# Optimization experiments

Measured on AMD Instinct MI355X. Metric: run time of the kernel, lower is better.

## Reference

```python
import jax, jax.numpy as jnp
import numpy as np

MIN_C = 1e-6
MIN_NORM = 1e-15
BALL_EPS = 0.004  # float32 ball epsilon


def _norm(x):
    return jnp.maximum(jnp.linalg.norm(x, axis=-1, keepdims=True), MIN_NORM)


def _project(x, c):
    norm = _norm(x)
    maxnorm = (1.0 - BALL_EPS) / jnp.sqrt(c)
    return jnp.where(norm > maxnorm, x / norm * maxnorm, x)


def _tanh(x):
    return jnp.tanh(jnp.clip(x, -15.0, 15.0))


def _artanh(x):
    x = jnp.clip(x, -1.0 + 1e-5, 1.0 - 1e-5)
    return 0.5 * (jnp.log1p(x) - jnp.log1p(-x))


def _expmap0(u, c):
    sc = jnp.sqrt(c)
    n = _norm(u)
    return _project(_tanh(sc * n) * u / (sc * n), c)


def _logmap0(y, c):
    sc = jnp.sqrt(c)
    n = _norm(y)
    return y / n / sc * _artanh(sc * n)


def _mobius_add(x, y, c):
    x2 = jnp.sum(x * x, -1, keepdims=True)
    y2 = jnp.sum(y * y, -1, keepdims=True)
    xy = jnp.sum(x * y, -1, keepdims=True)
    num = (1 + 2 * c * xy + c * y2) * x + (1 - c * x2) * y
    den = jnp.maximum(1 + 2 * c * xy + c * c * x2 * y2, MIN_NORM)
    return num / den


N_NODE, N_EDGE, D, ATTN, B, N_VOCAB = 100000, 1000000, 64, 64, 256, 401


def setup_inputs() -> dict:
    key = jax.random.key(0)
    ks = jax.random.split(key, 12)
    r_idx = jax.random.randint(ks[0], (N_EDGE,), 0, B, dtype=jnp.int32)
    rel = jax.random.randint(ks[1], (N_EDGE,), 0, N_VOCAB, dtype=jnp.int32)
    sub = jax.random.randint(ks[2], (N_EDGE,), 0, N_NODE, dtype=jnp.int32)
    obj = jax.random.randint(ks[3], (N_EDGE,), 0, N_NODE, dtype=jnp.int32)
    zero = jnp.zeros((N_EDGE,), jnp.int32)
    edges = jnp.stack([r_idx, zero, rel, zero, sub, obj], axis=1)  # [E, 6]
    s = 0.1
    return {
        "hidden": jax.random.normal(ks[4], (N_NODE, D), jnp.float32) * s,
        "q_rel": jax.random.randint(ks[5], (B,), 0, N_VOCAB, dtype=jnp.int32),
        "edges": edges,
        "rela_embed": jax.random.normal(ks[6], (N_VOCAB, D), jnp.float32) * s,
        "Ws_w": jax.random.normal(ks[7], (ATTN, D), jnp.float32) * s,
        "Wr_w": jax.random.normal(ks[8], (ATTN, D), jnp.float32) * s,
        "Wqr_w": jax.random.normal(ks[9], (ATTN, D), jnp.float32) * s,
        "Wqr_b": jnp.zeros((ATTN,), jnp.float32),
        "Wattn_w": jax.random.normal(ks[10], (1, ATTN), jnp.float32) * s,
        "Wh_w": jax.random.normal(ks[11], (D, D), jnp.float32) * s,
        "n_node": N_NODE,
    }


def reference(hidden, q_rel, edges, rela_embed, Ws_w, Wr_w, Wqr_w, Wqr_b, Wattn_w, Wh_w, n_node):
    c = MIN_C
    sub, rel, obj, r_idx = edges[:, 4], edges[:, 2], edges[:, 5], edges[:, 0]
    hs = hidden[sub]                 # [E, D] gather
    hr = rela_embed[rel]             # [E, D]
    h_qr = rela_embed[q_rel][r_idx]  # [E, D]
    # attention MLP -> scalar gate per edge
    pre = hs @ Ws_w.T + hr @ Wr_w.T + h_qr @ Wqr_w.T + Wqr_b
    alpha = jax.nn.sigmoid(jax.nn.relu(pre) @ Wattn_w.T)  # [E, 1]
    # hyperbolic message
    hs_h = _expmap0(hs, c)
    hr_h = _expmap0(hr, c)
    mess2 = _logmap0(_project(_mobius_add(hs_h, hr_h, c), c), c)
    message = mess2 * alpha
    agg = jax.ops.segment_sum(message, obj, num_segments=n_node)  # scatter-add
    a = _expmap0(agg @ Wh_w.T, c)
    a = jax.nn.relu(a)  # act
    return _logmap0(a, c)
```

## Files before the change

kernel.cpp:

```cpp
#include <hip/hip_runtime.h>
#include <math.h>
#include <stdint.h>

#define N_NODE 100000
#define N_EDGE 1000000
#define DIM    64
#define NB     256
#define NVOCAB 401
#define SCAN_B 1024
#define NCHUNK ((N_NODE + SCAN_B - 1) / SCAN_B)
#define AGG_WAVES 8192
#define NSHARD 8
#define EPB 2048

typedef short short8  __attribute__((ext_vector_type(8)));
typedef float floatx4 __attribute__((ext_vector_type(4)));
typedef unsigned short ushort_t;

__device__ inline unsigned short f2bf_rne(float f)
{
    unsigned u = __float_as_uint(f);
    unsigned r = u + 0x7FFF + ((u >> 16) & 1);
    return (unsigned short)(r >> 16);
}
__device__ inline float bflo(unsigned u) { return __uint_as_float(u << 16); }
__device__ inline float bfhi(unsigned u) { return __uint_as_float(u & 0xFFFF0000u); }
__device__ inline unsigned short f2h(float f)
{
    _Float16 h = (_Float16)f;
    unsigned short s; __builtin_memcpy(&s, &h, 2); return s;
}
__device__ inline float h2f(unsigned b)
{
    unsigned short s = (unsigned short)b;
    _Float16 h; __builtin_memcpy(&h, &s, 2); return (float)h;
}

__device__ inline void split8(float4 v0, float4 v1, short8& hi, short8& lo)
{
    float f[8] = {v0.x, v0.y, v0.z, v0.w, v1.x, v1.y, v1.z, v1.w};
    #pragma unroll
    for (int j = 0; j < 8; ++j) {
        unsigned u = __float_as_uint(f[j]);
        unsigned r = u + 0x7FFF + ((u >> 16) & 1);
        unsigned short h = (unsigned short)(r >> 16);
        float hf = __uint_as_float(((unsigned)h) << 16);
        float l  = f[j] - hf;
        unsigned u2 = __float_as_uint(l);
        unsigned r2 = u2 + 0x7FFF + ((u2 >> 16) & 1);
        hi[j] = (short)h;
        lo[j] = (short)(r2 >> 16);
    }
}

#define INIT_GRID ((NSHARD * N_NODE + 255) / 256)

__global__ __launch_bounds__(256) void init_kernel(
    const float* __restrict__ Ws, const float* __restrict__ Wr,
    const float* __restrict__ Wqr, const float* __restrict__ Wh,
    ushort_t* __restrict__ wsp, int* __restrict__ deg8)
{
    int tid = blockIdx.x * 256 + threadIdx.x;
    if (tid < NSHARD * N_NODE) deg8[tid] = 0;
    if (tid < 4 * 4096) {
        int w = tid >> 12, e = tid & 4095;
        const float* src = (w == 0) ? Ws : (w == 1) ? Wr : (w == 2) ? Wqr : Wh;
        float f = src[e];
        unsigned u = __float_as_uint(f);
        unsigned r = u + 0x7FFF + ((u >> 16) & 1);
        unsigned short h = (unsigned short)(r >> 16);
        float hf = __uint_as_float(((unsigned)h) << 16);
        float l  = f - hf;
        unsigned u2 = __float_as_uint(l);
        unsigned r2 = u2 + 0x7FFF + ((u2 >> 16) & 1);
        wsp[w * 8192 + e]        = h;
        wsp[w * 8192 + 4096 + e] = (unsigned short)(r2 >> 16);
    }
}

__device__ void gemm64p_body(
    const float* __restrict__ X,
    const int*   __restrict__ idx,
    const ushort_t* __restrict__ Whi,
    const ushort_t* __restrict__ Wlo,
    const float* __restrict__ bias,
    void* __restrict__ Yv,
    ushort_t* __restrict__ Y2,
    int R, int out_mode, int blk)
{
    int wave = threadIdx.x >> 6;
    int lane = threadIdx.x & 63;
    int m    = lane & 15;
    int quad = lane >> 4;
    int r0   = blk * 64 + wave * 16;

    int r = r0 + m;
    int src = (r < R) ? (idx ? idx[r] : r) : 0;
    const float* xrow = X + (size_t)src * DIM + quad * 8;

    float4 a0[2], a1[2];
    #pragma unroll
    for (int c = 0; c < 2; ++c) {
        a0[c] = *(const float4*)(xrow + 32 * c);
        a1[c] = *(const float4*)(xrow + 32 * c + 4);
    }
    short8 ah[2], al[2];
    #pragma unroll
    for (int c = 0; c < 2; ++c) split8(a0[c], a1[c], ah[c], al[c]);

    if (out_mode == 3 && r < R) {
        #pragma unroll
        for (int c = 0; c < 2; ++c)
            *(short8*)(Y2 + (size_t)r * DIM + 32 * c + quad * 8) = ah[c];
    }

    floatx4 acc[4] = {{0,0,0,0},{0,0,0,0},{0,0,0,0},{0,0,0,0}};
    #pragma unroll
    for (int g = 0; g < 4; ++g) {
        const ushort_t* whrow = Whi + (size_t)(g * 16 + m) * DIM + quad * 8;
        const ushort_t* wlrow = Wlo + (size_t)(g * 16 + m) * DIM + quad * 8;
        #pragma unroll
        for (int c = 0; c < 2; ++c) {
            short8 bh = *(const short8*)(whrow + 32 * c);
            short8 bl = *(const short8*)(wlrow + 32 * c);
            acc[g] = __builtin_amdgcn_mfma_f32_16x16x32_bf16(bh, ah[c], acc[g], 0, 0, 0);
            acc[g] = __builtin_amdgcn_mfma_f32_16x16x32_bf16(bl, ah[c], acc[g], 0, 0, 0);
            acc[g] = __builtin_amdgcn_mfma_f32_16x16x32_bf16(bh, al[c], acc[g], 0, 0, 0);
        }
    }

    if (r < R) {
        #pragma unroll
        for (int g = 0; g < 4; ++g) {
            float4 bv = make_float4(0.f, 0.f, 0.f, 0.f);
            if (bias) bv = *(const float4*)(bias + g * 16 + quad * 4);
            float v0 = acc[g][0] + bv.x;
            float v1 = acc[g][1] + bv.y;
            float v2 = acc[g][2] + bv.z;
            float v3 = acc[g][3] + bv.w;
            if (out_mode == 1) {
                v0 = fmaxf(v0, 0.f); v1 = fmaxf(v1, 0.f);
                v2 = fmaxf(v2, 0.f); v3 = fmaxf(v3, 0.f);
            }
            if (out_mode >= 2) {
                uint2 o;
                o.x = (unsigned)f2bf_rne(v0) | ((unsigned)f2bf_rne(v1) << 16);
                o.y = (unsigned)f2bf_rne(v2) | ((unsigned)f2bf_rne(v3) << 16);
                *(uint2*)((ushort_t*)Yv + (size_t)r * DIM + g * 16 + quad * 4) = o;
            } else {
                *(float4*)((float*)Yv + (size_t)r * DIM + g * 16 + quad * 4) =
                    make_float4(v0, v1, v2, v3);
            }
        }
    }
}

__global__ __launch_bounds__(256) void gemm64p_bf16A_kernel(
    const ushort_t* __restrict__ A,
    const ushort_t* __restrict__ Whi,
    const ushort_t* __restrict__ Wlo,
    float* __restrict__ Y, int R)
{
    int wave = threadIdx.x >> 6;
    int lane = threadIdx.x & 63;
    int m    = lane & 15;
    int quad = lane >> 4;
    int r0   = blockIdx.x * 64 + wave * 16;

    int r = r0 + m;
    int src = (r < R) ? r : 0;
    short8 a8[2];
    #pragma unroll
    for (int c = 0; c < 2; ++c)
        a8[c] = *(const short8*)(A + (size_t)src * DIM + 32 * c + quad * 8);

    floatx4 acc[4] = {{0,0,0,0},{0,0,0,0},{0,0,0,0},{0,0,0,0}};
    #pragma unroll
    for (int g = 0; g < 4; ++g) {
        const ushort_t* whrow = Whi + (size_t)(g * 16 + m) * DIM + quad * 8;
        const ushort_t* wlrow = Wlo + (size_t)(g * 16 + m) * DIM + quad * 8;
        #pragma unroll
        for (int c = 0; c < 2; ++c) {
            short8 bh = *(const short8*)(whrow + 32 * c);
            short8 bl = *(const short8*)(wlrow + 32 * c);
            acc[g] = __builtin_amdgcn_mfma_f32_16x16x32_bf16(bh, a8[c], acc[g], 0, 0, 0);
            acc[g] = __builtin_amdgcn_mfma_f32_16x16x32_bf16(bl, a8[c], acc[g], 0, 0, 0);
        }
    }

    if (r < R) {
        #pragma unroll
        for (int g = 0; g < 4; ++g) {
            *(float4*)(Y + (size_t)r * DIM + g * 16 + quad * 4) =
                make_float4(fmaxf(acc[g][0], 0.f), fmaxf(acc[g][1], 0.f),
                            fmaxf(acc[g][2], 0.f), fmaxf(acc[g][3], 0.f));
        }
    }
}

__device__ void gemm64_body(
    const float* __restrict__ X,
    const int*   __restrict__ idx,
    const float* __restrict__ W,
    const float* __restrict__ bias,
    void* __restrict__ Yv,
    ushort_t* __restrict__ Y2,
    int R, int out_mode, int blk)
{
    int wave = threadIdx.x >> 6;
    int lane = threadIdx.x & 63;
    int m    = lane & 15;
    int quad = lane >> 4;
    int r0   = blk * 64 + wave * 16;

    int r = r0 + m;
    int src = (r < R) ? (idx ? idx[r] : r) : 0;
    const float* xrow = X + (size_t)src * DIM + quad * 8;

    float4 a0[2], a1[2];
    #pragma unroll
    for (int c = 0; c < 2; ++c) {
        a0[c] = *(const float4*)(xrow + 32 * c);
        a1[c] = *(const float4*)(xrow + 32 * c + 4);
    }
    short8 ah[2], al[2];
    #pragma unroll
    for (int c = 0; c < 2; ++c) split8(a0[c], a1[c], ah[c], al[c]);

    if (out_mode == 3 && r < R) {
        #pragma unroll
        for (int c = 0; c < 2; ++c)
            *(short8*)(Y2 + (size_t)r * DIM + 32 * c + quad * 8) = ah[c];
    }

    floatx4 acc[4] = {{0,0,0,0},{0,0,0,0},{0,0,0,0},{0,0,0,0}};
    #pragma unroll
    for (int g = 0; g < 4; ++g) {
        const float* wrow = W + (size_t)(g * 16 + m) * DIM + quad * 8;
        #pragma unroll
        for (int c = 0; c < 2; ++c) {
            float4 b0 = *(const float4*)(wrow + 32 * c);
            float4 b1 = *(const float4*)(wrow + 32 * c + 4);
            short8 bh, bl;
            split8(b0, b1, bh, bl);
            acc[g] = __builtin_amdgcn_mfma_f32_16x16x32_bf16(ah[c], bh, acc[g], 0, 0, 0);
            acc[g] = __builtin_amdgcn_mfma_f32_16x16x32_bf16(ah[c], bl, acc[g], 0, 0, 0);
            acc[g] = __builtin_amdgcn_mfma_f32_16x16x32_bf16(al[c], bh, acc[g], 0, 0, 0);
        }
    }

    #pragma unroll
    for (int g = 0; g < 4; ++g) {
        float bv = bias ? bias[g * 16 + m] : 0.0f;
        #pragma unroll
        for (int reg = 0; reg < 4; ++reg) {
            int rr = r0 + quad * 4 + reg;
            if (rr < R) {
                float v = acc[g][reg] + bv;
                if (out_mode == 1) v = fmaxf(v, 0.0f);
                if (out_mode >= 2)
                    ((ushort_t*)Yv)[(size_t)rr * DIM + g * 16 + m] = f2bf_rne(v);
                else
                    ((float*)Yv)[(size_t)rr * DIM + g * 16 + m] = v;
            }
        }
    }
}

__global__ __launch_bounds__(256) void gemm64_kernel(
    const float* __restrict__ X, const int* __restrict__ idx,
    const float* __restrict__ W, const float* __restrict__ bias,
    void* __restrict__ Yv, ushort_t* __restrict__ Y2, int R, int out_mode)
{
    gemm64_body(X, idx, W, bias, Yv, Y2, R, out_mode, blockIdx.x);
}

#define G1 ((N_NODE + 63) / 64)
#define G2 ((NVOCAB + 63) / 64)
#define G3 (NB / 64)
#define GSMALL (G2 + G3)
#define GD8 ((N_EDGE + EPB - 1) / EPB)
#define PREP_T (G1 + GD8)
#define PREP_GRID (GSMALL + PREP_T)

__global__ __launch_bounds__(256) void prep_kernel(
    const float* __restrict__ hidden,
    const float* __restrict__ rela,
    const int*   __restrict__ q_rel,
    const ushort_t* __restrict__ wsp,
    const float* __restrict__ Wqr_b,
    ushort_t* __restrict__ hsWs,
    ushort_t* __restrict__ hidb,
    ushort_t* __restrict__ rel_preb,
    ushort_t* __restrict__ relab,
    ushort_t* __restrict__ qr_preb,
    const int* __restrict__ edges,
    int* __restrict__ deg8,
    int2* __restrict__ epack)
{
    int b = blockIdx.x;
    if (b < G2) {
        gemm64p_body(rela, nullptr, wsp + 1 * 8192, wsp + 1 * 8192 + 4096,
                     nullptr, rel_preb, relab, NVOCAB, 3, b);
    } else if (b < GSMALL) {
        gemm64p_body(rela, q_rel, wsp + 2 * 8192, wsp + 2 * 8192 + 4096,
                     Wqr_b, qr_preb, nullptr, NB, 2, b - G2);
    } else {
        int bp = b - GSMALL;
        int prior = (int)(((long)bp * GD8) / PREP_T);
        int nxt   = (int)(((long)(bp + 1) * GD8) / PREP_T);
        if (nxt > prior) {
            int base = prior * EPB + threadIdx.x;
            #pragma unroll
            for (int k = 0; k < 8; ++k) {
                int e = base + k * 256;
                if (e < N_EDGE) {
                    int2 ab = *(const int2*)(edges + (size_t)e * 6);
                    int2 cd = *(const int2*)(edges + (size_t)e * 6 + 2);
                    int2 ef = *(const int2*)(edges + (size_t)e * 6 + 4);
                    epack[e] = make_int2(ef.x | (cd.x << 17), ef.y | (ab.x << 17));
                    int s = (e >> 11) & (NSHARD - 1);
                    atomicAdd(&deg8[s * N_NODE + ef.y], 1);
                }
            }
        } else {
            gemm64p_body(hidden, nullptr, wsp, wsp + 4096,
                         nullptr, hsWs, hidb, N_NODE, 3, bp - prior);
        }
    }
}

__global__ __launch_bounds__(SCAN_B) void scan1_kernel(const int* __restrict__ deg8,
                                                       int* __restrict__ partial)
{
    __shared__ int s[SCAN_B];
    int g = blockIdx.x * SCAN_B + threadIdx.x;
    int tot = 0;
    if (g < N_NODE)
        #pragma unroll
        for (int k = 0; k < NSHARD; ++k) tot += deg8[k * N_NODE + g];
    s[threadIdx.x] = tot;
    __syncthreads();
    for (int off = SCAN_B / 2; off; off >>= 1) {
        if (threadIdx.x < off) s[threadIdx.x] += s[threadIdx.x + off];
        __syncthreads();
    }
    if (threadIdx.x == 0) partial[blockIdx.x] = s[0];
}

__global__ __launch_bounds__(SCAN_B) void scan3_kernel(int* __restrict__ deg8,
                                                       const int* __restrict__ partial,
                                                       int* __restrict__ offs)
{
    __shared__ int s[SCAN_B];
    __shared__ int pbase_s;
    int pb = (threadIdx.x < (int)blockIdx.x) ? partial[threadIdx.x] : 0;
    s[threadIdx.x] = pb;
    __syncthreads();
    for (int off = SCAN_B / 2; off; off >>= 1) {
        if (threadIdx.x < off) s[threadIdx.x] += s[threadIdx.x + off];
        __syncthreads();
    }
    if (threadIdx.x == 0) pbase_s = s[0];
    __syncthreads();
    int pbase = pbase_s;
    __syncthreads();

    int g = blockIdx.x * SCAN_B + threadIdx.x;
    int d[NSHARD];
    int tot = 0;
    if (g < N_NODE) {
        #pragma unroll
        for (int k = 0; k < NSHARD; ++k) { d[k] = deg8[k * N_NODE + g]; tot += d[k]; }
    }
    s[threadIdx.x] = tot;
    __syncthreads();
    for (int off = 1; off < SCAN_B; off <<= 1) {
        int add = ((int)threadIdx.x >= off) ? s[threadIdx.x - off] : 0;
        __syncthreads();
        s[threadIdx.x] += add;
        __syncthreads();
    }
    if (g < N_NODE) {
        int incl = pbase + s[threadIdx.x];
        offs[g + 1] = incl;
        if (g == 0) offs[0] = 0;
        int run = incl - tot;
        #pragma unroll
        for (int k = 0; k < NSHARD; ++k) { deg8[k * N_NODE + g] = run; run += d[k]; }
    }
}

__global__ __launch_bounds__(256) void alpha_scatter_kernel(
    const int2*     __restrict__ epack,
    int*            __restrict__ base8,
    const ushort_t* __restrict__ hsWs,
    const ushort_t* __restrict__ rel_preb,
    const ushort_t* __restrict__ qr_preb,
    const float*    __restrict__ wattn,
    int2*           __restrict__ csr2)
{
    int tid = blockIdx.x * 256 + threadIdx.x;
    if (tid < 32) csr2[N_EDGE + tid] = make_int2(0, 0);

    int wave = threadIdx.x >> 6;
    int lane = threadIdx.x & 63;
    int q    = lane >> 4;
    int l    = lane & 15;
    int f0   = l * 4;
    int e0   = (blockIdx.x * 4 + wave) * 16 + q * 4;

    float4 wa = *(const float4*)(wattn + f0);

    int   sub[4], rl[4], ob[4];
    float t[4];
    #pragma unroll
    for (int j = 0; j < 4; ++j) {
        int e = e0 + j;
        int2 ep = epack[e];
        sub[j] = ep.x & 0x1FFFF;
        rl[j]  = (int)((unsigned)ep.x >> 17);
        ob[j]  = ep.y & 0x1FFFF;
        int ri = (int)((unsigned)ep.y >> 17);

        uint2 uh = *(const uint2*)(hsWs     + (size_t)sub[j] * DIM + f0);
        uint2 ur = *(const uint2*)(rel_preb + (size_t)rl[j]  * DIM + f0);
        uint2 uq = *(const uint2*)(qr_preb  + (size_t)ri     * DIM + f0);

        float tt =  fmaxf(bflo(uh.x) + bflo(ur.x) + bflo(uq.x), 0.f) * wa.x;
        tt = fmaf(fmaxf(bfhi(uh.x) + bfhi(ur.x) + bfhi(uq.x), 0.f), wa.y, tt);
        tt = fmaf(fmaxf(bflo(uh.y) + bflo(ur.y) + bflo(uq.y), 0.f), wa.z, tt);
        tt = fmaf(fmaxf(bfhi(uh.y) + bfhi(ur.y) + bfhi(uq.y), 0.f), wa.w, tt);
        t[j] = tt;
    }
    #pragma unroll
    for (int j = 0; j < 4; ++j) {
        t[j] += __shfl_xor(t[j], 1);
        t[j] += __shfl_xor(t[j], 2);
        t[j] += __shfl_xor(t[j], 4);
        t[j] += __shfl_xor(t[j], 8);
    }

    if (l < 4) {
        int j = l;
        int sh = (e0 >> 11) & (NSHARD - 1);
        float alpha = 1.0f / (1.0f + __expf(-t[j]));
        int slot = atomicAdd(&base8[sh * N_NODE + ob[j]], 1);
        csr2[slot] = make_int2(sub[j],
            (int)(((unsigned)rl[j] << 16) | f2h(alpha)));
    }
}

__global__ __launch_bounds__(256) void agg_kernel(
    const int2*     __restrict__ csr2,
    const int*      __restrict__ offs,
    const ushort_t* __restrict__ hB,
    const ushort_t* __restrict__ relab,
    ushort_t* __restrict__ aggb)
{
    int lane = threadIdx.x & 63;
    int q    = lane >> 4;
    int l    = lane & 15;
    int f0   = l * 4;
    int wv = __builtin_amdgcn_readfirstlane((blockIdx.x * blockDim.x + threadIdx.x) >> 6);

    int i   = offs[wv];
    int end = offs[wv + 1];
    for (int n = wv; n < N_NODE; n += AGG_WAVES) {
        int nn = n + AGG_WAVES;
        int ni = 0, ne = 0;
        if (nn < N_NODE) { ni = offs[nn]; ne = offs[nn + 1]; }

        float4 acc = make_float4(0.f, 0.f, 0.f, 0.f);
        int2 e[4];
        #pragma unroll
        for (int j = 0; j < 4; ++j) e[j] = csr2[i + 4 * j + q];
        while (i < end) {
            int2 p[4];
            #pragma unroll
            for (int j = 0; j < 4; ++j) p[j] = csr2[i + 16 + 4 * j + q];

            uint2 uh[4], ur[4];
            #pragma unroll
            for (int j = 0; j < 4; ++j) {
                unsigned ey = (unsigned)e[j].y;
                uh[j] = *(const uint2*)(hB    + (((unsigned)e[j].x) << 6) + f0);
                ur[j] = *(const uint2*)(relab + ((ey >> 16) << 6) + f0);
            }
            #pragma unroll
            for (int j = 0; j < 4; ++j) {
                unsigned ey = (unsigned)e[j].y;
                float v  = (i + 4 * j + q < end) ? 1.0f : 0.0f;
                float al = v * h2f(ey & 0xFFFFu);
                acc.x = fmaf(al, bflo(uh[j].x) + bflo(ur[j].x), acc.x);
                acc.y = fmaf(al, bfhi(uh[j].x) + bfhi(ur[j].x), acc.y);
                acc.z = fmaf(al, bflo(uh[j].y) + bflo(ur[j].y), acc.z);
                acc.w = fmaf(al, bfhi(uh[j].y) + bfhi(ur[j].y), acc.w);
            }
            #pragma unroll
            for (int j = 0; j < 4; ++j) e[j] = p[j];
            i += 16;
        }

        acc.x += __shfl_xor(acc.x, 16); acc.x += __shfl_xor(acc.x, 32);
        acc.y += __shfl_xor(acc.y, 16); acc.y += __shfl_xor(acc.y, 32);
        acc.z += __shfl_xor(acc.z, 16); acc.z += __shfl_xor(acc.z, 32);
        acc.w += __shfl_xor(acc.w, 16); acc.w += __shfl_xor(acc.w, 32);
        if (q == 0) {
            uint2 o;
            o.x = (unsigned)f2bf_rne(acc.x) | ((unsigned)f2bf_rne(acc.y) << 16);
            o.y = (unsigned)f2bf_rne(acc.z) | ((unsigned)f2bf_rne(acc.w) << 16);
            *(uint2*)(aggb + (((unsigned)n) << 6) + f0) = o;
        }

        i = ni; end = ne;
    }
}

__global__ __launch_bounds__(256) void edge_kernel(
    const int*      __restrict__ edges,
    const ushort_t* __restrict__ hB,
    const ushort_t* __restrict__ relab,
    const ushort_t* __restrict__ hsWs,
    const ushort_t* __restrict__ rel_preb,
    const ushort_t* __restrict__ qr_preb,
    const float*    __restrict__ wattn,
    float* __restrict__ out)
{
    int e = (blockIdx.x * blockDim.x + threadIdx.x) >> 6;
    if (e >= N_EDGE) return;
    int lane = threadIdx.x & 63;
    int r_i = edges[e * 6 + 0];
    int rl  = edges[e * 6 + 2];
    int sb  = edges[e * 6 + 4];
    int ob  = edges[e * 6 + 5];
    float hs = __uint_as_float(((unsigned)hB[(size_t)sb * DIM + lane]) << 16);
    float hr = __uint_as_float(((unsigned)relab[(size_t)rl * DIM + lane]) << 16);
    float p1 = __uint_as_float(((unsigned)hsWs[(size_t)sb * DIM + lane]) << 16);
    float p2 = __uint_as_float(((unsigned)rel_preb[(size_t)rl * DIM + lane]) << 16);
    float p3 = __uint_as_float(((unsigned)qr_preb[(size_t)r_i * DIM + lane]) << 16);
    float t = wattn[lane] * fmaxf(p1 + p2 + p3, 0.0f);
    #pragma unroll
    for (int off = 32; off; off >>= 1) t += __shfl_xor(t, off);
    float alpha = 1.0f / (1.0f + __expf(-t));
    atomicAdd(&out[(size_t)ob * DIM + lane], (hs + hr) * alpha);
}

extern "C" void kernel_launch(void* const* d_in, const int* in_sizes, int n_in,
                              void* d_out, int out_size, void* d_ws, size_t ws_size,
                              hipStream_t stream)
{
    const float* hidden = (const float*)d_in[0];
    const int*   q_rel  = (const int*)  d_in[1];
    const int*   edges  = (const int*)  d_in[2];
    const float* rela   = (const float*)d_in[3];
    const float* Ws     = (const float*)d_in[4];
    const float* Wr     = (const float*)d_in[5];
    const float* Wqr    = (const float*)d_in[6];
    const float* Wqr_b  = (const float*)d_in[7];
    const float* Wattn  = (const float*)d_in[8];
    const float* Wh     = (const float*)d_in[9];
    float* out = (float*)d_out;

    ushort_t* qr_preb  = (ushort_t*)d_ws;
    ushort_t* rel_preb = qr_preb + NB * DIM;
    ushort_t* relab    = rel_preb + NVOCAB * DIM;
    ushort_t* hsWs     = relab + NVOCAB * DIM;
    ushort_t* hidb     = hsWs + (size_t)N_NODE * DIM;
    int2* epack  = (int2*)(((uintptr_t)(hidb + (size_t)N_NODE * DIM) + 15) & ~(uintptr_t)15);
    int*  rank   = (int*)(epack + N_EDGE);
    int*  deg8   = rank + N_EDGE;
    int*  offs   = deg8 + NSHARD * N_NODE;
    int*  partial= offs + (N_NODE + 1);
    int2* csr2   = (int2*)(((uintptr_t)(partial + 128) + 15) & ~(uintptr_t)15);
    ushort_t* wsp = (ushort_t*)(csr2 + N_EDGE + 32);
    size_t csr_need = ((char*)(wsp + 4 * 8192)) - (char*)d_ws;
    bool use_csr = ws_size >= csr_need;
    ushort_t* aggb = (ushort_t*)epack;

    if (use_csr) {
        init_kernel<<<INIT_GRID, 256, 0, stream>>>(Ws, Wr, Wqr, Wh, wsp, deg8);
        prep_kernel<<<PREP_GRID, 256, 0, stream>>>(
            hidden, rela, q_rel, wsp, Wqr_b,
            hsWs, hidb, rel_preb, relab, qr_preb, edges, deg8, epack);
        scan1_kernel<<<NCHUNK, SCAN_B, 0, stream>>>(deg8, partial);
        scan3_kernel<<<NCHUNK, SCAN_B, 0, stream>>>(deg8, partial, offs);
        alpha_scatter_kernel<<<N_EDGE / 64, 256, 0, stream>>>(
            epack, deg8, hsWs, rel_preb, qr_preb, Wattn, csr2);
        agg_kernel<<<AGG_WAVES / 4, 256, 0, stream>>>(csr2, offs, hidb, relab, aggb);
        gemm64p_bf16A_kernel<<<(N_NODE + 63) / 64, 256, 0, stream>>>(
            aggb, wsp + 3 * 8192, wsp + 3 * 8192 + 4096, out, N_NODE);
    } else {
        gemm64_kernel<<<(NVOCAB + 63) / 64, 256, 0, stream>>>(
            rela, nullptr, Wr, nullptr, rel_preb, relab, NVOCAB, 3);
        gemm64_kernel<<<(NB + 63) / 64, 256, 0, stream>>>(
            rela, q_rel, Wqr, Wqr_b, qr_preb, nullptr, NB, 2);
        gemm64_kernel<<<(N_NODE + 63) / 64, 256, 0, stream>>>(
            hidden, nullptr, Ws, nullptr, hsWs, hidb, N_NODE, 3);
        hipMemsetAsync(d_out, 0, (size_t)N_NODE * DIM * sizeof(float), stream);
        edge_kernel<<<(N_EDGE + 3) / 4, 256, 0, stream>>>(
            edges, hidb, relab, hsWs, rel_preb, qr_preb, Wattn, out);
        gemm64_kernel<<<(N_NODE + 63) / 64, 256, 0, stream>>>(
            out, nullptr, Wh, nullptr, out, nullptr, N_NODE, 1);
    }
}
```

Measured before the change: 261.1 us.

## Replace per-node CSR with 128-node bucket sort and LDS atomic aggregation

Edges are now counted into per-chunk histograms over 782 buckets of 128 destination nodes, replacing the per-node degree array spread over 8 shards. A three-pass scan turns these into per-chunk bucket offsets, and edges are scattered with LDS-local atomics instead of global atomics on a degree array. Aggregation runs one block per bucket and accumulates into a padded 128x65 LDS tile with shared-memory float atomics. This removes the global degree zeroing, the global atomic contention and the per-node wave scheduling. In exchange it adds LDS atomic traffic, and a block with a heavy bucket can run long, so load may be uneven across blocks.

```diff
diff --git a/kernel.cpp b/kernel.cpp
--- a/kernel.cpp
+++ b/kernel.cpp
@@ -7,11 +7,12 @@
 #define DIM    64
 #define NB     256
 #define NVOCAB 401
-#define SCAN_B 1024
-#define NCHUNK ((N_NODE + SCAN_B - 1) / SCAN_B)
-#define AGG_WAVES 8192
-#define NSHARD 8
-#define EPB 2048
+
+#define NBKT   782
+#define CHKE   1024
+#define NCHK   ((N_EDGE + CHKE - 1) / CHKE)
+#define SCAN_TOT (NBKT * NCHK)
+#define SCANA_GRID ((SCAN_TOT + 1023) / 1024)
 
 typedef short short8  __attribute__((ext_vector_type(8)));
 typedef float floatx4 __attribute__((ext_vector_type(4)));
@@ -53,15 +54,14 @@
     }
 }
 
-#define INIT_GRID ((NSHARD * N_NODE + 255) / 256)
+#define INIT_GRID ((4 * 4096 + 255) / 256)
 
 __global__ __launch_bounds__(256) void init_kernel(
     const float* __restrict__ Ws, const float* __restrict__ Wr,
     const float* __restrict__ Wqr, const float* __restrict__ Wh,
-    ushort_t* __restrict__ wsp, int* __restrict__ deg8)
+    ushort_t* __restrict__ wsp)
 {
     int tid = blockIdx.x * 256 + threadIdx.x;
-    if (tid < NSHARD * N_NODE) deg8[tid] = 0;
     if (tid < 4 * 4096) {
         int w = tid >> 12, e = tid & 4095;
         const float* src = (w == 0) ? Ws : (w == 1) ? Wr : (w == 2) ? Wqr : Wh;
@@ -279,11 +279,9 @@
 #define G2 ((NVOCAB + 63) / 64)
 #define G3 (NB / 64)
 #define GSMALL (G2 + G3)
-#define GD8 ((N_EDGE + EPB - 1) / EPB)
-#define PREP_T (G1 + GD8)
-#define PREP_GRID (GSMALL + PREP_T)
-
-__global__ __launch_bounds__(256) void prep_kernel(
+#define PREPC_GRID (NCHK + GSMALL + G1)
+
+__global__ __launch_bounds__(256) void prepcount_kernel(
     const float* __restrict__ hidden,
     const float* __restrict__ rela,
     const int*   __restrict__ q_rel,
@@ -295,225 +293,235 @@
     ushort_t* __restrict__ relab,
     ushort_t* __restrict__ qr_preb,
     const int* __restrict__ edges,
-    int* __restrict__ deg8,
-    int2* __restrict__ epack)
+    int2* __restrict__ epack,
+    int* __restrict__ histBB)
 {
     int b = blockIdx.x;
-    if (b < G2) {
+    if (b < NCHK) {
+        __shared__ unsigned cnt[NBKT];
+        for (int t = threadIdx.x; t < NBKT; t += 256) cnt[t] = 0;
+        __syncthreads();
+        int base = b * CHKE + threadIdx.x;
+        #pragma unroll
+        for (int k = 0; k < 4; ++k) {
+            int e = base + k * 256;
+            if (e < N_EDGE) {
+                int2 ab = *(const int2*)(edges + (size_t)e * 6);
+                int2 cd = *(const int2*)(edges + (size_t)e * 6 + 2);
+                int2 ef = *(const int2*)(edges + (size_t)e * 6 + 4);
+                epack[e] = make_int2(ef.x | (cd.x << 17), ef.y | (ab.x << 17));
+                atomicAdd(&cnt[ef.y >> 7], 1u);
+            }
+        }
+        __syncthreads();
+        for (int t = threadIdx.x; t < NBKT; t += 256)
+            histBB[b * NBKT + t] = (int)cnt[t];
+    } else if (b < NCHK + G2) {
         gemm64p_body(rela, nullptr, wsp + 1 * 8192, wsp + 1 * 8192 + 4096,
-                     nullptr, rel_preb, relab, NVOCAB, 3, b);
-    } else if (b < GSMALL) {
+                     nullptr, rel_preb, relab, NVOCAB, 3, b - NCHK);
+    } else if (b < NCHK + GSMALL) {
         gemm64p_body(rela, q_rel, wsp + 2 * 8192, wsp + 2 * 8192 + 4096,
-                     Wqr_b, qr_preb, nullptr, NB, 2, b - G2);
+                     Wqr_b, qr_preb, nullptr, NB, 2, b - NCHK - G2);
     } else {
-        int bp = b - GSMALL;
-        int prior = (int)(((long)bp * GD8) / PREP_T);
-        int nxt   = (int)(((long)(bp + 1) * GD8) / PREP_T);
-        if (nxt > prior) {
-            int base = prior * EPB + threadIdx.x;
-            #pragma unroll
-            for (int k = 0; k < 8; ++k) {
-                int e = base + k * 256;
-                if (e < N_EDGE) {
-                    int2 ab = *(const int2*)(edges + (size_t)e * 6);
-                    int2 cd = *(const int2*)(edges + (size_t)e * 6 + 2);
-                    int2 ef = *(const int2*)(edges + (size_t)e * 6 + 4);
-                    epack[e] = make_int2(ef.x | (cd.x << 17), ef.y | (ab.x << 17));
-                    int s = (e >> 11) & (NSHARD - 1);
-                    atomicAdd(&deg8[s * N_NODE + ef.y], 1);
-                }
-            }
-        } else {
-            gemm64p_body(hidden, nullptr, wsp, wsp + 4096,
-                         nullptr, hsWs, hidb, N_NODE, 3, bp - prior);
-        }
-    }
-}
-
-__global__ __launch_bounds__(SCAN_B) void scan1_kernel(const int* __restrict__ deg8,
-                                                       int* __restrict__ partial)
-{
-    __shared__ int s[SCAN_B];
-    int g = blockIdx.x * SCAN_B + threadIdx.x;
-    int tot = 0;
-    if (g < N_NODE)
-        #pragma unroll
-        for (int k = 0; k < NSHARD; ++k) tot += deg8[k * N_NODE + g];
-    s[threadIdx.x] = tot;
+        gemm64p_body(hidden, nullptr, wsp, wsp + 4096,
+                     nullptr, hsWs, hidb, N_NODE, 3, b - NCHK - GSMALL);
+    }
+}
+
+__global__ __launch_bounds__(1024) void scanA_kernel(
+    const int* __restrict__ histBB, int* __restrict__ offs2,
+    int* __restrict__ partialA)
+{
+    __shared__ int s[1024];
+    int t = threadIdx.x;
+    int m = blockIdx.x * 1024 + t;
+    int v = 0;
+    if (m < SCAN_TOT) {
+        int bin = m / NCHK, ch = m - bin * NCHK;
+        v = histBB[ch * NBKT + bin];
+    }
+    s[t] = v;
     __syncthreads();
-    for (int off = SCAN_B / 2; off; off >>= 1) {
-        if (threadIdx.x < off) s[threadIdx.x] += s[threadIdx.x + off];
+    for (int off = 1; off < 1024; off <<= 1) {
+        int add = (t >= off) ? s[t - off] : 0;
         __syncthreads();
-    }
-    if (threadIdx.x == 0) partial[blockIdx.x] = s[0];
-}
-
-__global__ __launch_bounds__(SCAN_B) void scan3_kernel(int* __restrict__ deg8,
-                                                       const int* __restrict__ partial,
-                                                       int* __restrict__ offs)
-{
-    __shared__ int s[SCAN_B];
-    __shared__ int pbase_s;
-    int pb = (threadIdx.x < (int)blockIdx.x) ? partial[threadIdx.x] : 0;
-    s[threadIdx.x] = pb;
+        s[t] += add;
+        __syncthreads();
+    }
+    if (m < SCAN_TOT) offs2[m] = s[t] - v;
+    if (t == 1023) partialA[blockIdx.x] = s[1023];
+}
+
+__global__ __launch_bounds__(1024) void scanB_kernel(
+    int* __restrict__ partialA, int* __restrict__ bstart)
+{
+    __shared__ int s[1024];
+    int t = threadIdx.x;
+    int v = (t < SCANA_GRID) ? partialA[t] : 0;
+    s[t] = v;
     __syncthreads();
-    for (int off = SCAN_B / 2; off; off >>= 1) {
-        if (threadIdx.x < off) s[threadIdx.x] += s[threadIdx.x + off];
+    for (int off = 1; off < 1024; off <<= 1) {
+        int add = (t >= off) ? s[t - off] : 0;
         __syncthreads();
-    }
-    if (threadIdx.x == 0) pbase_s = s[0];
-    __syncthreads();
-    int pbase = pbase_s;
-    __syncthreads();
-
-    int g = blockIdx.x * SCAN_B + threadIdx.x;
-    int d[NSHARD];
-    int tot = 0;
-    if (g < N_NODE) {
-        #pragma unroll
-        for (int k = 0; k < NSHARD; ++k) { d[k] = deg8[k * N_NODE + g]; tot += d[k]; }
-    }
-    s[threadIdx.x] = tot;
-    __syncthreads();
-    for (int off = 1; off < SCAN_B; off <<= 1) {
-        int add = ((int)threadIdx.x >= off) ? s[threadIdx.x - off] : 0;
+        s[t] += add;
         __syncthreads();
-        s[threadIdx.x] += add;
-        __syncthreads();
-    }
-    if (g < N_NODE) {
-        int incl = pbase + s[threadIdx.x];
-        offs[g + 1] = incl;
-        if (g == 0) offs[0] = 0;
-        int run = incl - tot;
-        #pragma unroll
-        for (int k = 0; k < NSHARD; ++k) { deg8[k * N_NODE + g] = run; run += d[k]; }
+    }
+    if (t < SCANA_GRID) partialA[t] = s[t] - v;
+    if (t == 0) bstart[NBKT] = N_EDGE;
+}
+
+__global__ __launch_bounds__(1024) void scanC_kernel(
+    int* __restrict__ offs2, const int* __restrict__ partialA,
+    int* __restrict__ bstart)
+{
+    int m = blockIdx.x * 1024 + threadIdx.x;
+    if (m < SCAN_TOT) {
+        int val = offs2[m] + partialA[blockIdx.x];
+        offs2[m] = val;
+        int bin = m / NCHK, ch = m - bin * NCHK;
+        if (ch == 0) bstart[bin] = val;
     }
 }
 
 __global__ __launch_bounds__(256) void alpha_scatter_kernel(
     const int2*     __restrict__ epack,
-    int*            __restrict__ base8,
+    const int*      __restrict__ offs2,
     const ushort_t* __restrict__ hsWs,
     const ushort_t* __restrict__ rel_preb,
     const ushort_t* __restrict__ qr_preb,
     const float*    __restrict__ wattn,
     int2*           __restrict__ csr2)
 {
-    int tid = blockIdx.x * 256 + threadIdx.x;
-    if (tid < 32) csr2[N_EDGE + tid] = make_int2(0, 0);
+    __shared__ int offL[NBKT];
+    int blk = blockIdx.x;
+    for (int t = threadIdx.x; t < NBKT; t += 256)
+        offL[t] = offs2[t * NCHK + blk];
+    if (blk == 0 && threadIdx.x < 32)
+        csr2[N_EDGE + threadIdx.x] = make_int2(0, 0);
+    __syncthreads();
 
     int wave = threadIdx.x >> 6;
     int lane = threadIdx.x & 63;
     int q    = lane >> 4;
     int l    = lane & 15;
     int f0   = l * 4;
-    int e0   = (blockIdx.x * 4 + wave) * 16 + q * 4;
-
     float4 wa = *(const float4*)(wattn + f0);
 
-    int   sub[4], rl[4], ob[4];
-    float t[4];
-    #pragma unroll
-    for (int j = 0; j < 4; ++j) {
-        int e = e0 + j;
-        int2 ep = epack[e];
-        sub[j] = ep.x & 0x1FFFF;
-        rl[j]  = (int)((unsigned)ep.x >> 17);
-        ob[j]  = ep.y & 0x1FFFF;
-        int ri = (int)((unsigned)ep.y >> 17);
-
-        uint2 uh = *(const uint2*)(hsWs     + (size_t)sub[j] * DIM + f0);
-        uint2 ur = *(const uint2*)(rel_preb + (size_t)rl[j]  * DIM + f0);
-        uint2 uq = *(const uint2*)(qr_preb  + (size_t)ri     * DIM + f0);
-
-        float tt =  fmaxf(bflo(uh.x) + bflo(ur.x) + bflo(uq.x), 0.f) * wa.x;
-        tt = fmaf(fmaxf(bfhi(uh.x) + bfhi(ur.x) + bfhi(uq.x), 0.f), wa.y, tt);
-        tt = fmaf(fmaxf(bflo(uh.y) + bflo(ur.y) + bflo(uq.y), 0.f), wa.z, tt);
-        tt = fmaf(fmaxf(bfhi(uh.y) + bfhi(ur.y) + bfhi(uq.y), 0.f), wa.w, tt);
-        t[j] = tt;
-    }
-    #pragma unroll
-    for (int j = 0; j < 4; ++j) {
-        t[j] += __shfl_xor(t[j], 1);
-        t[j] += __shfl_xor(t[j], 2);
-        t[j] += __shfl_xor(t[j], 4);
-        t[j] += __shfl_xor(t[j], 8);
-    }
-
-    if (l < 4) {
-        int j = l;
-        int sh = (e0 >> 11) & (NSHARD - 1);
-        float alpha = 1.0f / (1.0f + __expf(-t[j]));
-        int slot = atomicAdd(&base8[sh * N_NODE + ob[j]], 1);
-        csr2[slot] = make_int2(sub[j],
-            (int)(((unsigned)rl[j] << 16) | f2h(alpha)));
-    }
-}
+    for (int it = 0; it < 16; ++it) {
+        int e0 = blk * CHKE + wave * 256 + it * 16 + q * 4;
+
+        int   sub[4], rl[4], ob[4];
+        float tt[4];
+        #pragma unroll
+        for (int j = 0; j < 4; ++j) {
+            int e = e0 + j;
+            int2 ep = epack[min(e, N_EDGE - 1)];
+            sub[j] = ep.x & 0x1FFFF;
+            rl[j]  = (int)((unsigned)ep.x >> 17);
+            ob[j]  = ep.y & 0x1FFFF;
+            int ri = (int)((unsigned)ep.y >> 17);
+
+            uint2 uh = *(const uint2*)(hsWs     + (size_t)sub[j] * DIM + f0);
+            uint2 ur = *(const uint2*)(rel_preb + (size_t)rl[j]  * DIM + f0);
+            uint2 uq = *(const uint2*)(qr_preb  + (size_t)ri     * DIM + f0);
+
+            float s0 =  fmaxf(bflo(uh.x) + bflo(ur.x) + bflo(uq.x), 0.f) * wa.x;
+            s0 = fmaf(fmaxf(bfhi(uh.x) + bfhi(ur.x) + bfhi(uq.x), 0.f), wa.y, s0);
+            s0 = fmaf(fmaxf(bflo(uh.y) + bflo(ur.y) + bflo(uq.y), 0.f), wa.z, s0);
+            s0 = fmaf(fmaxf(bfhi(uh.y) + bfhi(ur.y) + bfhi(uq.y), 0.f), wa.w, s0);
+            tt[j] = s0;
+        }
+        #pragma unroll
+        for (int j = 0; j < 4; ++j) {
+            tt[j] += __shfl_xor(tt[j], 1);
+            tt[j] += __shfl_xor(tt[j], 2);
+            tt[j] += __shfl_xor(tt[j], 4);
+            tt[j] += __shfl_xor(tt[j], 8);
+        }
+
+        if (l < 4) {
+            int j = l;
+            int e = e0 + j;
+            if (e < N_EDGE) {
+                float alpha = 1.0f / (1.0f + __expf(-tt[j]));
+                int bin  = ob[j] >> 7;
+                int slot = atomicAdd(&offL[bin], 1);
+                csr2[slot] = make_int2(sub[j] | ((ob[j] & 127) << 17),
+                    (int)(((unsigned)rl[j] << 16) | f2h(alpha)));
+            }
+        }
+    }
+}
+
+#define AGG_LDSN (128 * 65)
 
 __global__ __launch_bounds__(256) void agg_kernel(
     const int2*     __restrict__ csr2,
-    const int*      __restrict__ offs,
+    const int*      __restrict__ bstart,
     const ushort_t* __restrict__ hB,
     const ushort_t* __restrict__ relab,
     ushort_t* __restrict__ aggb)
 {
+    __shared__ float accL[AGG_LDSN];
+    for (int t = threadIdx.x; t < AGG_LDSN; t += 256) accL[t] = 0.f;
+    __syncthreads();
+
+    int b = blockIdx.x;
+    int start = bstart[b];
+    int end   = bstart[b + 1];
+
+    int wave = threadIdx.x >> 6;
     int lane = threadIdx.x & 63;
     int q    = lane >> 4;
     int l    = lane & 15;
     int f0   = l * 4;
-    int wv = __builtin_amdgcn_readfirstlane((blockIdx.x * blockDim.x + threadIdx.x) >> 6);
-
-    int i   = offs[wv];
-    int end = offs[wv + 1];
-    for (int n = wv; n < N_NODE; n += AGG_WAVES) {
-        int nn = n + AGG_WAVES;
-        int ni = 0, ne = 0;
-        if (nn < N_NODE) { ni = offs[nn]; ne = offs[nn + 1]; }
-
-        float4 acc = make_float4(0.f, 0.f, 0.f, 0.f);
-        int2 e[4];
-        #pragma unroll
-        for (int j = 0; j < 4; ++j) e[j] = csr2[i + 4 * j + q];
-        while (i < end) {
-            int2 p[4];
-            #pragma unroll
-            for (int j = 0; j < 4; ++j) p[j] = csr2[i + 16 + 4 * j + q];
-
-            uint2 uh[4], ur[4];
-            #pragma unroll
-            for (int j = 0; j < 4; ++j) {
-                unsigned ey = (unsigned)e[j].y;
-                uh[j] = *(const uint2*)(hB    + (((unsigned)e[j].x) << 6) + f0);
-                ur[j] = *(const uint2*)(relab + ((ey >> 16) << 6) + f0);
-            }
-            #pragma unroll
-            for (int j = 0; j < 4; ++j) {
-                unsigned ey = (unsigned)e[j].y;
-                float v  = (i + 4 * j + q < end) ? 1.0f : 0.0f;
-                float al = v * h2f(ey & 0xFFFFu);
-                acc.x = fmaf(al, bflo(uh[j].x) + bflo(ur[j].x), acc.x);
-                acc.y = fmaf(al, bfhi(uh[j].x) + bfhi(ur[j].x), acc.y);
-                acc.z = fmaf(al, bflo(uh[j].y) + bflo(ur[j].y), acc.z);
-                acc.w = fmaf(al, bfhi(uh[j].y) + bfhi(ur[j].y), acc.w);
-            }
-            #pragma unroll
-            for (int j = 0; j < 4; ++j) e[j] = p[j];
-            i += 16;
-        }
-
-        acc.x += __shfl_xor(acc.x, 16); acc.x += __shfl_xor(acc.x, 32);
-        acc.y += __shfl_xor(acc.y, 16); acc.y += __shfl_xor(acc.y, 32);
-        acc.z += __shfl_xor(acc.z, 16); acc.z += __shfl_xor(acc.z, 32);
-        acc.w += __shfl_xor(acc.w, 16); acc.w += __shfl_xor(acc.w, 32);
-        if (q == 0) {
+
+    int i = start + wave * 16;
+    int2 e[4];
+    #pragma unroll
+    for (int j = 0; j < 4; ++j) e[j] = csr2[min(i + 4 * j + q, N_EDGE + 31)];
+    while (i < end) {
+        int2 p[4];
+        #pragma unroll
+        for (int j = 0; j < 4; ++j) p[j] = csr2[min(i + 64 + 4 * j + q, N_EDGE + 31)];
+
+        uint2 uh[4], ur[4];
+        #pragma unroll
+        for (int j = 0; j < 4; ++j) {
+            unsigned ex = (unsigned)e[j].x, ey = (unsigned)e[j].y;
+            uh[j] = *(const uint2*)(hB    + ((ex & 0x1FFFFu) << 6) + f0);
+            ur[j] = *(const uint2*)(relab + ((ey >> 16) << 6) + f0);
+        }
+        #pragma unroll
+        for (int j = 0; j < 4; ++j) {
+            unsigned ex = (unsigned)e[j].x, ey = (unsigned)e[j].y;
+            float v  = (i + 4 * j + q < end) ? 1.0f : 0.0f;
+            float al = v * h2f(ey & 0xFFFFu);
+            float* row = &accL[(ex >> 17) * 65 + f0];
+            atomicAdd(&row[0], al * (bflo(uh[j].x) + bflo(ur[j].x)));
+            atomicAdd(&row[1], al * (bfhi(uh[j].x) + bfhi(ur[j].x)));
+            atomicAdd(&row[2], al * (bflo(uh[j].y) + bflo(ur[j].y)));
+            atomicAdd(&row[3], al * (bfhi(uh[j].y) + bfhi(ur[j].y)));
+        }
+        #pragma unroll
+        for (int j = 0; j < 4; ++j) e[j] = p[j];
+        i += 64;
+    }
+    __syncthreads();
+
+    int t15 = threadIdx.x & 15;
+    int rr0 = threadIdx.x >> 4;
+    #pragma unroll
+    for (int it = 0; it < 8; ++it) {
+        int r = it * 16 + rr0;
+        int n = b * 128 + r;
+        if (n < N_NODE) {
+            const float* rowp = &accL[r * 65 + t15 * 4];
             uint2 o;
-            o.x = (unsigned)f2bf_rne(acc.x) | ((unsigned)f2bf_rne(acc.y) << 16);
-            o.y = (unsigned)f2bf_rne(acc.z) | ((unsigned)f2bf_rne(acc.w) << 16);
-            *(uint2*)(aggb + (((unsigned)n) << 6) + f0) = o;
-        }
-
-        i = ni; end = ne;
+            o.x = (unsigned)f2bf_rne(rowp[0]) | ((unsigned)f2bf_rne(rowp[1]) << 16);
+            o.y = (unsigned)f2bf_rne(rowp[2]) | ((unsigned)f2bf_rne(rowp[3]) << 16);
+            *(uint2*)(aggb + ((size_t)n << 6) + t15 * 4) = o;
+        }
     }
 }
 
@@ -568,26 +576,27 @@
     ushort_t* hsWs     = relab + NVOCAB * DIM;
     ushort_t* hidb     = hsWs + (size_t)N_NODE * DIM;
     int2* epack  = (int2*)(((uintptr_t)(hidb + (size_t)N_NODE * DIM) + 15) & ~(uintptr_t)15);
-    int*  rank   = (int*)(epack + N_EDGE);
-    int*  deg8   = rank + N_EDGE;
-    int*  offs   = deg8 + NSHARD * N_NODE;
-    int*  partial= offs + (N_NODE + 1);
-    int2* csr2   = (int2*)(((uintptr_t)(partial + 128) + 15) & ~(uintptr_t)15);
+    int*  histBB = (int*)(epack + N_EDGE);
+    int*  offs2  = histBB + SCAN_TOT;
+    int*  partialA = offs2 + SCAN_TOT;
+    int*  bstart   = partialA + 1024;
+    int2* csr2   = (int2*)(((uintptr_t)(bstart + NBKT + 1) + 15) & ~(uintptr_t)15);
     ushort_t* wsp = (ushort_t*)(csr2 + N_EDGE + 32);
     size_t csr_need = ((char*)(wsp + 4 * 8192)) - (char*)d_ws;
     bool use_csr = ws_size >= csr_need;
     ushort_t* aggb = (ushort_t*)epack;
 
     if (use_csr) {
-        init_kernel<<<INIT_GRID, 256, 0, stream>>>(Ws, Wr, Wqr, Wh, wsp, deg8);
-        prep_kernel<<<PREP_GRID, 256, 0, stream>>>(
+        init_kernel<<<INIT_GRID, 256, 0, stream>>>(Ws, Wr, Wqr, Wh, wsp);
+        prepcount_kernel<<<PREPC_GRID, 256, 0, stream>>>(
             hidden, rela, q_rel, wsp, Wqr_b,
-            hsWs, hidb, rel_preb, relab, qr_preb, edges, deg8, epack);
-        scan1_kernel<<<NCHUNK, SCAN_B, 0, stream>>>(deg8, partial);
-        scan3_kernel<<<NCHUNK, SCAN_B, 0, stream>>>(deg8, partial, offs);
-        alpha_scatter_kernel<<<N_EDGE / 64, 256, 0, stream>>>(
-            epack, deg8, hsWs, rel_preb, qr_preb, Wattn, csr2);
-        agg_kernel<<<AGG_WAVES / 4, 256, 0, stream>>>(csr2, offs, hidb, relab, aggb);
+            hsWs, hidb, rel_preb, relab, qr_preb, edges, epack, histBB);
+        scanA_kernel<<<SCANA_GRID, 1024, 0, stream>>>(histBB, offs2, partialA);
+        scanB_kernel<<<1, 1024, 0, stream>>>(partialA, bstart);
+        scanC_kernel<<<SCANA_GRID, 1024, 0, stream>>>(offs2, partialA, bstart);
+        alpha_scatter_kernel<<<NCHK, 256, 0, stream>>>(
+            epack, offs2, hsWs, rel_preb, qr_preb, Wattn, csr2);
+        agg_kernel<<<NBKT, 256, 0, stream>>>(csr2, bstart, hidb, relab, aggb);
         gemm64p_bf16A_kernel<<<(N_NODE + 63) / 64, 256, 0, stream>>>(
             aggb, wsp + 3 * 8192, wsp + 3 * 8192 + 4096, out, N_NODE);
     } else {
```

Result: slower. 645.4 us (+147.2%).
